# Kernel tuning notes

Hardware: AMD Instinct MI355X
Metric: run time of the kernel (lower is better)

Reference implementation:

```python
import jax, jax.numpy as jnp
import numpy as np

B, C, H, W, Q = 4, 64, 48, 48, 16384
HID = 256
IN_DIM = 4 * C + 4  # 4 pyramid levels concat + rel_coord(2) + rel_cell(2)


def _conv(x, w, b, stride=1, pad=1):
    y = jax.lax.conv_general_dilated(x, w, (stride, stride), [(pad, pad), (pad, pad)],
                                     dimension_numbers=('NCHW', 'OIHW', 'NCHW'))
    return y + b[None, :, None, None]


def _pixel_shuffle(x, r=2):
    b, c, h, w = x.shape
    return x.reshape(b, c // (r * r), r, r, h, w).transpose(0, 1, 4, 2, 5, 3).reshape(b, c // (r * r), h * r, w * r)


def _gather(img, iy, ix):
    # img [B,C,H,W], iy/ix [B,Q] int -> [B,Q,C]
    return jax.vmap(lambda f, y, x: f[:, y, x].T)(img, iy, ix)


def _nearest_idx(coord, h, w):
    # PyTorch grid_sample nearest, align_corners=False: unnormalize then nearbyint
    iy = jnp.clip(jnp.round((coord[..., 0] + 1.0) * (h / 2.0) - 0.5), 0, h - 1).astype(jnp.int32)
    ix = jnp.clip(jnp.round((coord[..., 1] + 1.0) * (w / 2.0) - 0.5), 0, w - 1).astype(jnp.int32)
    return iy, ix


def _bilinear_border(img, coord):
    b, c, h, w = img.shape
    fy = jnp.clip((coord[..., 0] + 1.0) * (h / 2.0) - 0.5, 0.0, h - 1.0)
    fx = jnp.clip((coord[..., 1] + 1.0) * (w / 2.0) - 0.5, 0.0, w - 1.0)
    y0 = jnp.floor(fy); x0 = jnp.floor(fx)
    wy = (fy - y0)[..., None]; wx = (fx - x0)[..., None]
    y0i = y0.astype(jnp.int32); x0i = x0.astype(jnp.int32)
    y1i = jnp.clip(y0i + 1, 0, h - 1); x1i = jnp.clip(x0i + 1, 0, w - 1)
    v00 = _gather(img, y0i, x0i); v01 = _gather(img, y0i, x1i)
    v10 = _gather(img, y1i, x0i); v11 = _gather(img, y1i, x1i)
    return v00 * (1 - wy) * (1 - wx) + v01 * (1 - wy) * wx + v10 * wy * (1 - wx) + v11 * wy * wx


def _mlp(x, ws, bs):
    for wm, bm in zip(ws[:-1], bs[:-1]):
        x = jnp.maximum(x @ wm + bm, 0.0)
    return x @ ws[-1] + bs[-1]


def _forward(inp, coord, cell, enc_w, enc_b, up1_w, up1_b, up2_w, up2_b, up3_w, up3_b,
             skip1_w, skip1_b, skip2_w, skip2_b, down4_w, down4_b, down5_w, down5_b,
             mlp_ws, mlp_bs):
    feat = _conv(inp, enc_w, enc_b)                                   # [B,C,H,W]
    feat_1 = _pixel_shuffle(_conv(feat, up1_w, up1_b))                # [B,C,2H,2W]
    feat_2 = _pixel_shuffle(_conv(feat_1, up2_w, up2_b))              # [B,C,4H,4W]
    feat_3 = _pixel_shuffle(_conv(feat_2, up3_w, up3_b))              # [B,C,8H,8W]
    feat_4 = _conv(feat_3, down4_w, down4_b, stride=2) + _conv(feat_2, skip1_w, skip1_b, pad=0)
    feat_5 = _conv(feat_4, down5_w, down5_b, stride=2) + _conv(feat_1, skip2_w, skip2_b, pad=0)
    h, w = feat.shape[-2], feat.shape[-1]
    rx = 1.0 / h  # 2 / h / 2
    ry = 1.0 / w
    eps_shift = 1e-6
    scale = jnp.array([h, w], dtype=coord.dtype)
    rel_cell = cell * scale
    preds, areas = [], []
    for vx in (-1.0, 1.0):
        for vy in (-1.0, 1.0):
            shift = jnp.array([vx * rx + eps_shift, vy * ry + eps_shift], dtype=coord.dtype)
            coord_ = jnp.clip(coord + shift, -1 + 1e-6, 1 - 1e-6)
            iy, ix = _nearest_idx(coord_, h, w)
            q_feat = _gather(feat, iy, ix)
            i5y, i5x = _nearest_idx(coord_, feat_5.shape[-2], feat_5.shape[-1])
            q_feat2x = _gather(feat_5, i5y, i5x)
            i4y, i4x = _nearest_idx(coord_, feat_4.shape[-2], feat_4.shape[-1])
            q_feat4x = _gather(feat_4, i4y, i4x)
            i3y, i3x = _nearest_idx(coord_, feat_3.shape[-2], feat_3.shape[-1])
            q_feat8x = _gather(feat_3, i3y, i3x)
            # feat_coord holds cell-center coords; nearest-sampling it equals this closed form
            q_coord = jnp.stack([-1.0 + (2.0 * iy + 1.0) / h, -1.0 + (2.0 * ix + 1.0) / w],
                                axis=-1).astype(coord.dtype)
            rel_coord = (coord - q_coord) * scale
            x = jnp.concatenate([q_feat, q_feat2x, q_feat4x, q_feat8x, rel_coord, rel_cell], axis=-1)
            preds.append(_mlp(x, mlp_ws, mlp_bs))
            areas.append(jnp.abs(rel_coord[..., 0] * rel_coord[..., 1]) + 1e-9)
    tot_area = areas[0] + areas[1] + areas[2] + areas[3]
    areas = [areas[3], areas[2], areas[1], areas[0]]  # local-ensemble diagonal swap
    ret = sum(p * (a / tot_area)[..., None] for p, a in zip(preds, areas))
    ret = ret + _bilinear_border(inp, coord)
    return ret


def setup_inputs() -> dict:
    key = jax.random.key(0)
    ks = jax.random.split(key, 24)
    d = {}
    d['inp'] = jax.random.normal(ks[0], (B, 3, H, W), jnp.float32)
    d['coord'] = jax.random.uniform(ks[1], (B, Q, 2), jnp.float32, -1.0, 1.0)
    d['cell'] = jnp.full((B, Q, 2), 2.0 / (8 * H), jnp.float32)

    def conv_p(k, co, ci, kh):
        wkey, _ = jax.random.split(k)
        wgt = jax.random.normal(wkey, (co, ci, kh, kh), jnp.float32) * (1.0 / np.sqrt(ci * kh * kh))
        return wgt, jnp.zeros((co,), jnp.float32)

    d['enc_w'], d['enc_b'] = conv_p(ks[2], C, 3, 3)
    d['up1_w'], d['up1_b'] = conv_p(ks[3], 4 * C, C, 3)
    d['up2_w'], d['up2_b'] = conv_p(ks[4], 4 * C, C, 3)
    d['up3_w'], d['up3_b'] = conv_p(ks[5], 4 * C, C, 3)
    d['skip1_w'], d['skip1_b'] = conv_p(ks[6], C, C, 1)
    d['skip2_w'], d['skip2_b'] = conv_p(ks[7], C, C, 1)
    d['down4_w'], d['down4_b'] = conv_p(ks[8], C, C, 3)
    d['down5_w'], d['down5_b'] = conv_p(ks[9], C, C, 3)
    dims = [IN_DIM, HID, HID, HID, HID, 3]
    for i in range(5):
        d['mlp_w%d' % i] = jax.random.normal(ks[10 + i], (dims[i], dims[i + 1]), jnp.float32) * (1.0 / np.sqrt(dims[i]))
        d['mlp_b%d' % i] = jnp.zeros((dims[i + 1],), jnp.float32)
    return d


def reference(inp, coord, cell, enc_w, enc_b, up1_w, up1_b, up2_w, up2_b, up3_w, up3_b,
              skip1_w, skip1_b, skip2_w, skip2_b, down4_w, down4_b, down5_w, down5_b,
              mlp_w0, mlp_b0, mlp_w1, mlp_b1, mlp_w2, mlp_b2, mlp_w3, mlp_b3, mlp_w4, mlp_b4):
    mlp_ws = [mlp_w0, mlp_w1, mlp_w2, mlp_w3, mlp_w4]
    mlp_bs = [mlp_b0, mlp_b1, mlp_b2, mlp_b3, mlp_b4]
    return _forward(inp, coord, cell, enc_w, enc_b, up1_w, up1_b, up2_w, up2_b, up3_w, up3_b,
                    skip1_w, skip1_b, skip2_w, skip2_b, down4_w, down4_b, down5_w, down5_b,
                    mlp_ws, mlp_bs)
```

## Files before the change

### kernel.cpp

```cpp
#include <hip/hip_runtime.h>
#include <stdint.h>

typedef unsigned int u32;
typedef unsigned short u16;

#define DI __device__ __forceinline__

DI float bf2f(u16 h){ return __uint_as_float(((u32)h)<<16); }
DI u16 f2bf(float f){ u32 u = __float_as_uint(f); return (u16)((u + 0x7FFFu + ((u>>16)&1u))>>16); }
DI u32 pack2(float a, float b){ return (u32)f2bf(a) | ((u32)f2bf(b)<<16); }

typedef __attribute__((ext_vector_type(8))) short bf16x8;
typedef __attribute__((ext_vector_type(4))) float f32x4;

#define NIN 29
__device__ const int g_in_off[NIN] = {
  0,27648,158720,289792,291520,291584,439040,439296,586752,587008,734464,
  734720,738816,738880,742976,743040,779904,779968,816832,816896,883456,
  883712,949248,949504,1015040,1015296,1080832,1081088,1081856};
#define CVT_TOTAL 1081859

#define O_INP      0
#define O_COORD    27648
#define O_CELL     158720
#define O_ENCW     289792
#define O_ENCB     291520
#define O_UP1W     291584
#define O_UP1B     439040
#define O_UP2W     439296
#define O_UP2B     586752
#define O_UP3W     587008
#define O_UP3B     734464
#define O_SK1W     734720
#define O_SK1B     738816
#define O_SK2W     738880
#define O_SK2B     742976
#define O_DN4W     743040
#define O_DN4B     779904
#define O_DN5W     779968
#define O_DN5B     816832
#define O_MLPW0    816896
#define O_MLPB0    883456
#define O_MLPW1    883712
#define O_MLPB1    949248
#define O_MLPW2    949504
#define O_MLPB2    1015040
#define O_MLPW3    1015296
#define O_MLPB3    1080832
#define O_MLPW4    1081088
#define O_MLPB4    1081856

#define W_CVT    16
#define W_FRAG   1082000
#define FG_UP1 0
#define FG_UP2 147456
#define FG_UP3 294912
#define FG_D4  442368
#define FG_D5  483328
#define CONV_FRAG_TOTAL 524288
#define FG_MLP 524288
#define FO_L0 0
#define FO_L1 73728
#define FO_L2 139264
#define FO_L3 204800
#define FO_L4 270336
#define FRAG_TOTAL 274432
#define W_FEAT   1481360
#define W_FEAT1  1776272
#define W_FEAT2  2955920
#define W_FEAT3  7674512
#define W_FEAT4  26548880
#define W_FEAT5  31267472

#define AST 296

__global__ void k_detect(const void* cell, int* flag){
  if (threadIdx.x == 0 && blockIdx.x == 0){
    u32 u = *(const u32*)cell;
    *flag = ((u >> 16) == (u & 0xFFFFu)) ? 1 : 0;
  }
}

struct Ptrs { const void* p[NIN]; };

__global__ __launch_bounds__(256) void k_convert(Ptrs ptrs, const int* __restrict__ flag, float* __restrict__ dst){
  int idx = blockIdx.x*256 + threadIdx.x;
  if (idx >= CVT_TOTAL) return;
  int bf = *flag;
  int i = 0;
  #pragma unroll
  for (int s = 1; s < NIN; ++s) if (idx >= g_in_off[s]) i = s;
  int local = idx - g_in_off[i];
  float v;
  if (bf) v = bf2f(((const u16*)ptrs.p[i])[local]);
  else    v = ((const float*)ptrs.p[i])[local];
  dst[idx] = v;
}

__global__ __launch_bounds__(256) void k_repack_conv(const float* __restrict__ cvt, u16* __restrict__ dst){
  int idx = blockIdx.x*256 + threadIdx.x;
  float v;
  if (idx < 442368){
    int seg = idx / 147456, base = idx % 147456;
    const int wo[3] = {O_UP1W, O_UP2W, O_UP3W};
    int t = base & 511, c = base >> 9;
    int j = t & 7, lane = t >> 3;
    int col = lane & 15, quad = lane >> 4;
    int kc = c >> 4, rem = c & 15;
    int wv = rem >> 2, nt = rem & 3;
    int k = kc*32 + quad*8 + j;
    int kid = k >> 6, ci = k & 63;
    int co = (wv*16 + col)*4 + nt;
    v = cvt[wo[seg] + co*576 + ci*9 + kid];
  } else {
    int x = idx - 442368;
    int seg = x / 40960, base = x % 40960;
    int t = base & 511, c = base >> 9;
    int j = t & 7, lane = t >> 3;
    int col = lane & 15, quad = lane >> 4;
    int kc = c >> 2, nt = c & 3;
    int k = kc*32 + quad*8 + j;
    int co = nt*16 + col;
    if (k < 576){
      int kid = k >> 6, ci = k & 63;
      v = cvt[(seg ? O_DN5W : O_DN4W) + co*576 + ci*9 + kid];
    } else {
      int ci = k - 576;
      v = cvt[(seg ? O_SK2W : O_SK1W) + co*64 + ci];
    }
  }
  dst[idx] = f2bf(v);
}

__global__ __launch_bounds__(256) void k_repack_mlp(const float* __restrict__ cvt, u16* __restrict__ dst){
  int idx = blockIdx.x*256 + threadIdx.x;
  int l, base;
  if (idx < FO_L1)      { l = 0; base = idx; }
  else if (idx < FO_L2) { l = 1; base = idx - FO_L1; }
  else if (idx < FO_L3) { l = 2; base = idx - FO_L2; }
  else if (idx < FO_L4) { l = 3; base = idx - FO_L3; }
  else                  { l = 4; base = idx - FO_L4; }
  int t = base & 511, c = base >> 9;
  int L = t >> 3, j = t & 7;
  int ntiles = (l == 4) ? 1 : 16;
  int kc = c / ntiles, nt = c % ntiles;
  int k = kc*32 + (L>>4)*8 + j;
  int n = nt*16 + (L&15);
  const int srcw[5] = {O_MLPW0, O_MLPW1, O_MLPW2, O_MLPW3, O_MLPW4};
  int Kvalid = (l == 0) ? 260 : 256;
  int N = (l == 4) ? 3 : 256;
  float v = 0.f;
  if (k < Kvalid && n < N) v = cvt[srcw[l] + k*N + n];
  dst[idx] = f2bf(v);
}

__global__ __launch_bounds__(256) void k_enc(const float* __restrict__ cvt, u16* __restrict__ feat){
  int gid = blockIdx.x*256 + threadIdx.x;
  int co = gid & 63, pix = gid >> 6;
  int x = pix % 48; int t = pix / 48; int y = t % 48; int b = t / 48;
  const float* w = cvt + O_ENCW + co*27;
  float acc = cvt[O_ENCB + co];
  const float* ip = cvt + O_INP + b*3*2304;
  #pragma unroll
  for (int ci = 0; ci < 3; ++ci)
    for (int dy = 0; dy < 3; ++dy){
      int iy = y + dy - 1;
      for (int dx = 0; dx < 3; ++dx){
        int ix = x + dx - 1;
        float v = (iy>=0 && iy<48 && ix>=0 && ix<48) ? ip[ci*2304 + iy*48 + ix] : 0.f;
        acc = fmaf(w[ci*9 + dy*3 + dx], v, acc);
      }
    }
  feat[pix*64 + co] = f2bf(acc);
}

template<int H>
__global__ __launch_bounds__(256,2) void k_upconv_mfma(const u16* __restrict__ in,
    const u16* __restrict__ wf, const float* __restrict__ bias, u16* __restrict__ out){
  __shared__ __align__(16) u16 patch[100*72];
  const int TW = H/8;
  int b = blockIdx.y;
  int y0 = (blockIdx.x / TW)*8, x0 = (blockIdx.x % TW)*8;
  int tid = threadIdx.x;
  if (tid < 200){
    int p = tid >> 1, half = tid & 1;
    int pr = p/10, pc = p - pr*10;
    int gy = y0+pr-1, gx = x0+pc-1;
    uint4* dst = (uint4*)((char*)(patch + p*72) + half*64);
    if (gy>=0 && gy<H && gx>=0 && gx<H){
      const uint4* src = (const uint4*)((const char*)(in + ((b*H+gy)*H+gx)*64) + half*64);
      dst[0]=src[0]; dst[1]=src[1]; dst[2]=src[2]; dst[3]=src[3];
    } else {
      uint4 z = {0,0,0,0};
      dst[0]=z; dst[1]=z; dst[2]=z; dst[3]=z;
    }
  }
  __syncthreads();
  int lane = tid & 63, wv = __builtin_amdgcn_readfirstlane(tid>>6);
  int col = lane & 15, quad = lane >> 4;
  f32x4 acc[4][4];
  #pragma unroll
  for (int nt=0;nt<4;++nt){
    float bv = bias[(wv*16+col)*4+nt];
    #pragma unroll
    for (int mt=0;mt<4;++mt) acc[mt][nt] = (f32x4){bv,bv,bv,bv};
  }
  int pyc[4], pxc[4];
  #pragma unroll
  for (int mt=0;mt<4;++mt){ int p = mt*16+col; pyc[mt]=p>>3; pxc[mt]=p&7; }
  #pragma unroll
  for (int kc=0; kc<18; ++kc){
    int dydx = kc>>1, half = kc&1;
    int dy = dydx/3, dx = dydx%3;
    bf16x8 a[4], bb[4];
    #pragma unroll
    for (int mt=0;mt<4;++mt)
      a[mt] = *(const bf16x8*)(patch + ((pyc[mt]+dy)*10 + pxc[mt]+dx)*72 + half*32 + quad*8);
    #pragma unroll
    for (int nt=0;nt<4;++nt)
      bb[nt] = *(const bf16x8*)(wf + ((kc*16 + wv*4 + nt)*64 + lane)*8);
    #pragma unroll
    for (int mt=0;mt<4;++mt)
      #pragma unroll
      for (int nt=0;nt<4;++nt)
        acc[mt][nt] = __builtin_amdgcn_mfma_f32_16x16x32_bf16(a[mt], bb[nt], acc[mt][nt], 0,0,0);
  }
  const int W2 = 2*H;
  #pragma unroll
  for (int mt=0;mt<4;++mt)
    #pragma unroll
    for (int r=0;r<4;++r){
      int p = mt*16 + quad*4 + r;
      int oy = 2*(y0 + (p>>3)), ox = 2*(x0 + (p&7));
      #pragma unroll
      for (int nt=0;nt<4;++nt)
        out[((b*W2 + oy + (nt>>1))*W2 + ox + (nt&1))*64 + wv*16 + col] = f2bf(acc[mt][nt][r]);
    }
}

template<int HO>
__global__ __launch_bounds__(256,2) void k_down_mfma(const u16* __restrict__ in3,
    const u16* __restrict__ in2, const u16* __restrict__ wf,
    const float* __restrict__ biasd, const float* __restrict__ biass, u16* __restrict__ out){
  __shared__ __align__(16) u16 patch3[289*72];
  __shared__ __align__(16) u16 patch2[64*72];
  const int HI = 2*HO, TW = HO/8;
  int b = blockIdx.y;
  int y0 = (blockIdx.x / TW)*8, x0 = (blockIdx.x % TW)*8;
  int tid = threadIdx.x;
  for (int u = tid; u < 578; u += 256){
    int p = u >> 1, half = u & 1;
    int pr = p/17, pc = p - pr*17;
    int gy = 2*y0 - 1 + pr, gx = 2*x0 - 1 + pc;
    uint4* dst = (uint4*)((char*)(patch3 + p*72) + half*64);
    if (gy>=0 && gy<HI && gx>=0 && gx<HI){
      const uint4* src = (const uint4*)((const char*)(in3 + ((b*HI+gy)*HI+gx)*64) + half*64);
      dst[0]=src[0]; dst[1]=src[1]; dst[2]=src[2]; dst[3]=src[3];
    } else { uint4 z={0,0,0,0}; dst[0]=z; dst[1]=z; dst[2]=z; dst[3]=z; }
  }
  if (tid < 128){
    int p = tid >> 1, half = tid & 1;
    int gy = y0 + (p>>3), gx = x0 + (p&7);
    uint4* dst = (uint4*)((char*)(patch2 + p*72) + half*64);
    const uint4* src = (const uint4*)((const char*)(in2 + ((b*HO+gy)*HO+gx)*64) + half*64);
    dst[0]=src[0]; dst[1]=src[1]; dst[2]=src[2]; dst[3]=src[3];
  }
  __syncthreads();
  int lane = tid & 63, wv = __builtin_amdgcn_readfirstlane(tid>>6);
  int col = lane & 15, quad = lane >> 4;
  f32x4 acc[4];
  {
    float bv = biasd[wv*16+col] + biass[wv*16+col];
    #pragma unroll
    for (int mt=0;mt<4;++mt) acc[mt] = (f32x4){bv,bv,bv,bv};
  }
  int pyc[4], pxc[4];
  #pragma unroll
  for (int mt=0;mt<4;++mt){ int p = mt*16+col; pyc[mt]=p>>3; pxc[mt]=p&7; }
  #pragma unroll
  for (int kc=0; kc<20; ++kc){
    bf16x8 a[4];
    if (kc < 18){
      int dydx = kc>>1, half = kc&1;
      int dy = dydx/3, dx = dydx%3;
      #pragma unroll
      for (int mt=0;mt<4;++mt)
        a[mt] = *(const bf16x8*)(patch3 + ((2*pyc[mt]+dy)*17 + 2*pxc[mt]+dx)*72 + half*32 + quad*8);
    } else {
      #pragma unroll
      for (int mt=0;mt<4;++mt)
        a[mt] = *(const bf16x8*)(patch2 + (pyc[mt]*8+pxc[mt])*72 + (kc-18)*32 + quad*8);
    }
    bf16x8 bb = *(const bf16x8*)(wf + ((kc*4 + wv)*64 + lane)*8);
    #pragma unroll
    for (int mt=0;mt<4;++mt)
      acc[mt] = __builtin_amdgcn_mfma_f32_16x16x32_bf16(a[mt], bb, acc[mt], 0,0,0);
  }
  #pragma unroll
  for (int mt=0;mt<4;++mt)
    #pragma unroll
    for (int r=0;r<4;++r){
      int p = mt*16 + quad*4 + r;
      out[((b*HO + y0+(p>>3))*HO + x0+(p&7))*64 + wv*16+col] = f2bf(acc[mt][r]);
    }
}

DI void shifted_coord(float cy, float cx, int e, float& cy_, float& cx_){
  float vx = (e & 2) ? 1.f : -1.f;
  float vy = (e & 1) ? 1.f : -1.f;
  float sy = (float)((double)vx*(1.0/48.0) + 1e-6);
  float sx = (float)((double)vy*(1.0/48.0) + 1e-6);
  const float clo = (float)(-1.0 + 1e-6), chi = (float)(1.0 - 1e-6);
  cy_ = fminf(fmaxf(__fadd_rn(cy, sy), clo), chi);
  cx_ = fminf(fmaxf(__fadd_rn(cx, sx), clo), chi);
}
DI int nidx(float c_, int hL){
  float f = __fadd_rn(__fmul_rn(__fadd_rn(c_, 1.f), (float)hL*0.5f), -0.5f);
  int i = (int)rintf(f);
  return max(0, min(hL-1, i));
}

template<int KC>
DI void layer_compute(const u16* __restrict__ Ab, const u16* __restrict__ wf,
                      const float* __restrict__ bias, int lane, int wv, f32x4 (&acc)[4][4]){
  int col = lane & 15, quad = lane >> 4;
  #pragma unroll
  for (int mt=0;mt<4;++mt)
    #pragma unroll
    for (int nt=0;nt<4;++nt){
      float bv = bias[wv*64 + nt*16 + col];
      acc[mt][nt] = (f32x4){bv,bv,bv,bv};
    }
  for (int kc=0; kc<KC; ++kc){
    bf16x8 a[4], b[4];
    #pragma unroll
    for (int mt=0;mt<4;++mt)
      a[mt] = *(const bf16x8*)(Ab + (mt*16+col)*AST + kc*32 + quad*8);
    #pragma unroll
    for (int nt=0;nt<4;++nt)
      b[nt] = *(const bf16x8*)(wf + ((kc*16 + wv*4 + nt)*64 + lane)*8);
    #pragma unroll
    for (int mt=0;mt<4;++mt)
      #pragma unroll
      for (int nt=0;nt<4;++nt)
        acc[mt][nt] = __builtin_amdgcn_mfma_f32_16x16x32_bf16(a[mt], b[nt], acc[mt][nt], 0, 0, 0);
  }
}

DI void layer_store(u16* __restrict__ Ab, f32x4 (&acc)[4][4], int lane, int wv){
  int col = lane & 15, quad = lane >> 4;
  #pragma unroll
  for (int mt=0;mt<4;++mt)
    #pragma unroll
    for (int nt=0;nt<4;++nt)
      #pragma unroll
      for (int r=0;r<4;++r)
        Ab[(mt*16 + quad*4 + r)*AST + wv*64 + nt*16 + col] = f2bf(fmaxf(acc[mt][nt][r], 0.f));
}

__global__ __launch_bounds__(256) void k_query(const float* __restrict__ cvt,
    const u16* __restrict__ feat, const u16* __restrict__ feat3,
    const u16* __restrict__ feat4, const u16* __restrict__ feat5,
    const u16* __restrict__ wfrag, const int* __restrict__ flagp, void* __restrict__ outv){
  __shared__ __align__(16) u16 Abuf[64*AST];
  __shared__ float predbuf[64*3];
  int tid = threadIdx.x;

  {
    int r = tid >> 2, part = tid & 3;
    int gq = blockIdx.x*16 + (r>>2);
    int e = r & 3;
    int b = gq >> 14, q = gq & 16383;
    float cy = cvt[O_COORD + (b*16384+q)*2 + 0];
    float cx = cvt[O_COORD + (b*16384+q)*2 + 1];
    float cy_, cx_; shifted_coord(cy, cx, e, cy_, cx_);
    int hL = (part==0) ? 48 : (part==1) ? 96 : (part==2) ? 192 : 384;
    const u16* fp = (part==0) ? feat : (part==1) ? feat5 : (part==2) ? feat4 : feat3;
    int iy = nidx(cy_, hL), ix = nidx(cx_, hL);
    const uint4* src = (const uint4*)(fp + ((b*hL + iy)*hL + ix)*64);
    uint4* dst = (uint4*)((char*)Abuf + r*(AST*2) + part*128);
    #pragma unroll
    for (int i=0;i<8;++i) dst[i] = src[i];
  }
  if (tid < 64){
    int gq = blockIdx.x*16 + (tid>>2);
    int e = tid & 3;
    int b = gq >> 14, q = gq & 16383;
    float cy = cvt[O_COORD + (b*16384+q)*2 + 0];
    float cx = cvt[O_COORD + (b*16384+q)*2 + 1];
    float cy_, cx_; shifted_coord(cy, cx, e, cy_, cx_);
    int iy = nidx(cy_, 48), ix = nidx(cx_, 48);
    float qy = -1.f + (2.f*iy + 1.f)*(1.f/48.f);
    float qx = -1.f + (2.f*ix + 1.f)*(1.f/48.f);
    float r0 = (cy - qy)*48.f;
    float r1 = (cx - qx)*48.f;
    float r2 = cvt[O_CELL + (b*16384+q)*2 + 0]*48.f;
    float r3 = cvt[O_CELL + (b*16384+q)*2 + 1]*48.f;
    u32* dst = (u32*)((char*)Abuf + tid*(AST*2) + 512);
    dst[0] = pack2(r0, r1);
    dst[1] = pack2(r2, r3);
    #pragma unroll
    for (int z=0; z<14; ++z) dst[2+z] = 0u;
  }
  __syncthreads();

  int lane = tid & 63;
  int wv = __builtin_amdgcn_readfirstlane(tid >> 6);

  { f32x4 acc[4][4];
    layer_compute<9>(Abuf, wfrag + FO_L0, cvt + O_MLPB0, lane, wv, acc);
    __syncthreads(); layer_store(Abuf, acc, lane, wv); }
  __syncthreads();
  { f32x4 acc[4][4];
    layer_compute<8>(Abuf, wfrag + FO_L1, cvt + O_MLPB1, lane, wv, acc);
    __syncthreads(); layer_store(Abuf, acc, lane, wv); }
  __syncthreads();
  { f32x4 acc[4][4];
    layer_compute<8>(Abuf, wfrag + FO_L2, cvt + O_MLPB2, lane, wv, acc);
    __syncthreads(); layer_store(Abuf, acc, lane, wv); }
  __syncthreads();
  { f32x4 acc[4][4];
    layer_compute<8>(Abuf, wfrag + FO_L3, cvt + O_MLPB3, lane, wv, acc);
    __syncthreads(); layer_store(Abuf, acc, lane, wv); }
  __syncthreads();

  {
    int col = lane & 15, quad = lane >> 4;
    float bv = (col < 3) ? cvt[O_MLPB4 + col] : 0.f;
    f32x4 a4 = (f32x4){bv,bv,bv,bv};
    for (int kc=0; kc<8; ++kc){
      bf16x8 av = *(const bf16x8*)(Abuf + (wv*16 + col)*AST + kc*32 + quad*8);
      bf16x8 bv8 = *(const bf16x8*)(wfrag + FO_L4 + (kc*64 + lane)*8);
      a4 = __builtin_amdgcn_mfma_f32_16x16x32_bf16(av, bv8, a4, 0, 0, 0);
    }
    if (col < 3){
      #pragma unroll
      for (int r=0;r<4;++r)
        predbuf[(wv*16 + quad*4 + r)*3 + col] = a4[r];
    }
  }
  __syncthreads();

  if (tid < 16){
    int gq = blockIdx.x*16 + tid;
    int b = gq >> 14, q = gq & 16383;
    float cy = cvt[O_COORD + (b*16384+q)*2 + 0];
    float cx = cvt[O_COORD + (b*16384+q)*2 + 1];
    float a[4];
    #pragma unroll
    for (int e=0;e<4;++e){
      float cy_, cx_; shifted_coord(cy, cx, e, cy_, cx_);
      int iy = nidx(cy_, 48), ix = nidx(cx_, 48);
      float qy = -1.f + (2.f*iy + 1.f)*(1.f/48.f);
      float qx = -1.f + (2.f*ix + 1.f)*(1.f/48.f);
      float ry = (cy - qy)*48.f, rx = (cx - qx)*48.f;
      a[e] = fabsf(ry*rx) + 1e-9f;
    }
    float tot = a[0]+a[1]+a[2]+a[3];
    float fy = fminf(fmaxf((cy+1.f)*24.f - 0.5f, 0.f), 47.f);
    float fx = fminf(fmaxf((cx+1.f)*24.f - 0.5f, 0.f), 47.f);
    float y0f = floorf(fy), x0f = floorf(fx);
    float wy = fy - y0f, wx = fx - x0f;
    int y0 = (int)y0f, x0 = (int)x0f;
    int y1 = min(y0+1, 47), x1 = min(x0+1, 47);
    int bf = *flagp;
    #pragma unroll
    for (int ch=0; ch<3; ++ch){
      const float* ip = cvt + O_INP + (b*3 + ch)*2304;
      float v00 = ip[y0*48+x0], v01 = ip[y0*48+x1], v10 = ip[y1*48+x0], v11 = ip[y1*48+x1];
      float v = v00*(1.f-wy)*(1.f-wx) + v01*(1.f-wy)*wx + v10*wy*(1.f-wx) + v11*wy*wx;
      #pragma unroll
      for (int e=0;e<4;++e)
        v += predbuf[(tid*4+e)*3 + ch] * (a[3-e]/tot);
      int oi = (b*16384+q)*3 + ch;
      if (bf) ((u16*)outv)[oi] = f2bf(v);
      else    ((float*)outv)[oi] = v;
    }
  }
}

extern "C" void kernel_launch(void* const* d_in, const int* in_sizes, int n_in,
                              void* d_out, int out_size, void* d_ws, size_t ws_size,
                              hipStream_t stream){
  float* ws = (float*)d_ws;
  int* flag = (int*)d_ws;
  float* cvt = ws + W_CVT;
  u16* frag = (u16*)(ws + W_FRAG);
  u16* feat  = (u16*)(ws + W_FEAT);
  u16* feat1 = (u16*)(ws + W_FEAT1);
  u16* feat2 = (u16*)(ws + W_FEAT2);
  u16* feat3 = (u16*)(ws + W_FEAT3);
  u16* feat4 = (u16*)(ws + W_FEAT4);
  u16* feat5 = (u16*)(ws + W_FEAT5);
  Ptrs ptrs;
  for (int i = 0; i < NIN && i < n_in; ++i) ptrs.p[i] = d_in[i];

  k_detect<<<1, 64, 0, stream>>>(d_in[2], flag);
  k_convert<<<(CVT_TOTAL+255)/256, 256, 0, stream>>>(ptrs, flag, cvt);
  k_repack_conv<<<CONV_FRAG_TOTAL/256, 256, 0, stream>>>(cvt, frag);
  k_repack_mlp<<<FRAG_TOTAL/256, 256, 0, stream>>>(cvt, frag + FG_MLP);
  k_enc<<<2304, 256, 0, stream>>>(cvt, feat);
  k_upconv_mfma<48> <<<dim3(36, 4), 256, 0, stream>>>(feat,  frag+FG_UP1, cvt+O_UP1B, feat1);
  k_upconv_mfma<96> <<<dim3(144,4), 256, 0, stream>>>(feat1, frag+FG_UP2, cvt+O_UP2B, feat2);
  k_upconv_mfma<192><<<dim3(576,4), 256, 0, stream>>>(feat2, frag+FG_UP3, cvt+O_UP3B, feat3);
  k_down_mfma<192><<<dim3(576,4), 256, 0, stream>>>(feat3, feat2, frag+FG_D4, cvt+O_DN4B, cvt+O_SK1B, feat4);
  k_down_mfma<96> <<<dim3(144,4), 256, 0, stream>>>(feat4, feat1, frag+FG_D5, cvt+O_DN5B, cvt+O_SK2B, feat5);
  k_query<<<4096, 256, 0, stream>>>(cvt, feat, feat3, feat4, feat5, frag + FG_MLP, flag, d_out);
}
```

Baseline: 433.2 us.

## Switch query MLP hidden layers to 32x32x16 MFMA and merge repack kernels

The hidden layers of the per-query MLP now use 32x32x16 bf16 MFMA tiles (2x2 per wave) in place of 16x16x32 tiles (4x4 per wave), and the MLP weight fragment layout is repacked to match. This roughly halves the LDS A-fragment and global B-fragment loads per MFMA and cuts the instruction count. The conv and MLP repack kernels are merged into one launch to save a kernel launch. The risk is a different accumulator register footprint and a more scattered LDS store pattern in the new layer store.

```diff
diff --git a/kernel.cpp b/kernel.cpp
--- a/kernel.cpp
+++ b/kernel.cpp
@@ -12,6 +12,7 @@
 
 typedef __attribute__((ext_vector_type(8))) short bf16x8;
 typedef __attribute__((ext_vector_type(4))) float f32x4;
+typedef __attribute__((ext_vector_type(16))) float f32x16;
 
 #define NIN 29
 __device__ const int g_in_off[NIN] = {
@@ -65,6 +66,7 @@
 #define FO_L3 204800
 #define FO_L4 270336
 #define FRAG_TOTAL 274432
+#define REPACK_TOTAL (CONV_FRAG_TOTAL + FRAG_TOTAL)
 #define W_FEAT   1481360
 #define W_FEAT1  1776272
 #define W_FEAT2  2955920
@@ -97,7 +99,7 @@
   dst[idx] = v;
 }
 
-__global__ __launch_bounds__(256) void k_repack_conv(const float* __restrict__ cvt, u16* __restrict__ dst){
+__global__ __launch_bounds__(256) void k_repack_all(const float* __restrict__ cvt, u16* __restrict__ dst){
   int idx = blockIdx.x*256 + threadIdx.x;
   float v;
   if (idx < 442368){
@@ -112,7 +114,7 @@
     int kid = k >> 6, ci = k & 63;
     int co = (wv*16 + col)*4 + nt;
     v = cvt[wo[seg] + co*576 + ci*9 + kid];
-  } else {
+  } else if (idx < CONV_FRAG_TOTAL){
     int x = idx - 442368;
     int seg = x / 40960, base = x % 40960;
     int t = base & 511, c = base >> 9;
@@ -128,29 +130,31 @@
       int ci = k - 576;
       v = cvt[(seg ? O_SK2W : O_SK1W) + co*64 + ci];
     }
-  }
-  dst[idx] = f2bf(v);
-}
-
-__global__ __launch_bounds__(256) void k_repack_mlp(const float* __restrict__ cvt, u16* __restrict__ dst){
-  int idx = blockIdx.x*256 + threadIdx.x;
-  int l, base;
-  if (idx < FO_L1)      { l = 0; base = idx; }
-  else if (idx < FO_L2) { l = 1; base = idx - FO_L1; }
-  else if (idx < FO_L3) { l = 2; base = idx - FO_L2; }
-  else if (idx < FO_L4) { l = 3; base = idx - FO_L3; }
-  else                  { l = 4; base = idx - FO_L4; }
-  int t = base & 511, c = base >> 9;
-  int L = t >> 3, j = t & 7;
-  int ntiles = (l == 4) ? 1 : 16;
-  int kc = c / ntiles, nt = c % ntiles;
-  int k = kc*32 + (L>>4)*8 + j;
-  int n = nt*16 + (L&15);
-  const int srcw[5] = {O_MLPW0, O_MLPW1, O_MLPW2, O_MLPW3, O_MLPW4};
-  int Kvalid = (l == 0) ? 260 : 256;
-  int N = (l == 4) ? 3 : 256;
-  float v = 0.f;
-  if (k < Kvalid && n < N) v = cvt[srcw[l] + k*N + n];
+  } else {
+    int midx = idx - FG_MLP;
+    int l, base;
+    if (midx < FO_L1)      { l = 0; base = midx; }
+    else if (midx < FO_L2) { l = 1; base = midx - FO_L1; }
+    else if (midx < FO_L3) { l = 2; base = midx - FO_L2; }
+    else if (midx < FO_L4) { l = 3; base = midx - FO_L3; }
+    else                   { l = 4; base = midx - FO_L4; }
+    int t = base & 511, c = base >> 9;
+    int L = t >> 3, j = t & 7;
+    int k, n;
+    if (l < 4){
+      int kc = c >> 3, nt2 = c & 7;
+      k = kc*16 + (L>>5)*8 + j;
+      n = nt2*32 + (L&31);
+    } else {
+      k = c*32 + (L>>4)*8 + j;
+      n = L & 15;
+    }
+    const int srcw[5] = {O_MLPW0, O_MLPW1, O_MLPW2, O_MLPW3, O_MLPW4};
+    int Kvalid = (l == 0) ? 260 : 256;
+    int N = (l == 4) ? 3 : 256;
+    v = 0.f;
+    if (k < Kvalid && n < N) v = cvt[srcw[l] + k*N + n];
+  }
   dst[idx] = f2bf(v);
 }
 
@@ -320,42 +324,45 @@
   return max(0, min(hL-1, i));
 }
 
-template<int KC>
-DI void layer_compute(const u16* __restrict__ Ab, const u16* __restrict__ wf,
-                      const float* __restrict__ bias, int lane, int wv, f32x4 (&acc)[4][4]){
-  int col = lane & 15, quad = lane >> 4;
-  #pragma unroll
-  for (int mt=0;mt<4;++mt)
-    #pragma unroll
-    for (int nt=0;nt<4;++nt){
-      float bv = bias[wv*64 + nt*16 + col];
-      acc[mt][nt] = (f32x4){bv,bv,bv,bv};
-    }
-  for (int kc=0; kc<KC; ++kc){
-    bf16x8 a[4], b[4];
-    #pragma unroll
-    for (int mt=0;mt<4;++mt)
-      a[mt] = *(const bf16x8*)(Ab + (mt*16+col)*AST + kc*32 + quad*8);
-    #pragma unroll
-    for (int nt=0;nt<4;++nt)
-      b[nt] = *(const bf16x8*)(wf + ((kc*16 + wv*4 + nt)*64 + lane)*8);
-    #pragma unroll
-    for (int mt=0;mt<4;++mt)
-      #pragma unroll
-      for (int nt=0;nt<4;++nt)
-        acc[mt][nt] = __builtin_amdgcn_mfma_f32_16x16x32_bf16(a[mt], b[nt], acc[mt][nt], 0, 0, 0);
-  }
-}
-
-DI void layer_store(u16* __restrict__ Ab, f32x4 (&acc)[4][4], int lane, int wv){
-  int col = lane & 15, quad = lane >> 4;
-  #pragma unroll
-  for (int mt=0;mt<4;++mt)
-    #pragma unroll
-    for (int nt=0;nt<4;++nt)
-      #pragma unroll
-      for (int r=0;r<4;++r)
-        Ab[(mt*16 + quad*4 + r)*AST + wv*64 + nt*16 + col] = f2bf(fmaxf(acc[mt][nt][r], 0.f));
+template<int KC16>
+DI void layer_compute32(const u16* __restrict__ Ab, const u16* __restrict__ wf,
+                        const float* __restrict__ bias, int lane, int wv, f32x16 (&acc)[2][2]){
+  int col = lane & 31, half = lane >> 5;
+  #pragma unroll
+  for (int mt=0;mt<2;++mt)
+    #pragma unroll
+    for (int nt=0;nt<2;++nt){
+      float bv = bias[wv*64 + nt*32 + col];
+      #pragma unroll
+      for (int r=0;r<16;++r) acc[mt][nt][r] = bv;
+    }
+  for (int kc=0; kc<KC16; ++kc){
+    bf16x8 a[2], b[2];
+    #pragma unroll
+    for (int mt=0;mt<2;++mt)
+      a[mt] = *(const bf16x8*)(Ab + (mt*32+col)*AST + kc*16 + half*8);
+    #pragma unroll
+    for (int nt=0;nt<2;++nt)
+      b[nt] = *(const bf16x8*)(wf + ((kc*8 + wv*2 + nt)*64 + lane)*8);
+    #pragma unroll
+    for (int mt=0;mt<2;++mt)
+      #pragma unroll
+      for (int nt=0;nt<2;++nt)
+        acc[mt][nt] = __builtin_amdgcn_mfma_f32_32x32x16_bf16(a[mt], b[nt], acc[mt][nt], 0, 0, 0);
+  }
+}
+
+DI void layer_store32(u16* __restrict__ Ab, f32x16 (&acc)[2][2], int lane, int wv){
+  int col = lane & 31, half = lane >> 5;
+  #pragma unroll
+  for (int mt=0;mt<2;++mt)
+    #pragma unroll
+    for (int nt=0;nt<2;++nt)
+      #pragma unroll
+      for (int r=0;r<16;++r){
+        int row = mt*32 + (r&3) + 8*(r>>2) + 4*half;
+        Ab[row*AST + wv*64 + nt*32 + col] = f2bf(fmaxf(acc[mt][nt][r], 0.f));
+      }
 }
 
 __global__ __launch_bounds__(256) void k_query(const float* __restrict__ cvt,
@@ -407,21 +414,21 @@
   int lane = tid & 63;
   int wv = __builtin_amdgcn_readfirstlane(tid >> 6);
 
-  { f32x4 acc[4][4];
-    layer_compute<9>(Abuf, wfrag + FO_L0, cvt + O_MLPB0, lane, wv, acc);
-    __syncthreads(); layer_store(Abuf, acc, lane, wv); }
-  __syncthreads();
-  { f32x4 acc[4][4];
-    layer_compute<8>(Abuf, wfrag + FO_L1, cvt + O_MLPB1, lane, wv, acc);
-    __syncthreads(); layer_store(Abuf, acc, lane, wv); }
-  __syncthreads();
-  { f32x4 acc[4][4];
-    layer_compute<8>(Abuf, wfrag + FO_L2, cvt + O_MLPB2, lane, wv, acc);
-    __syncthreads(); layer_store(Abuf, acc, lane, wv); }
-  __syncthreads();
-  { f32x4 acc[4][4];
-    layer_compute<8>(Abuf, wfrag + FO_L3, cvt + O_MLPB3, lane, wv, acc);
-    __syncthreads(); layer_store(Abuf, acc, lane, wv); }
+  { f32x16 acc[2][2];
+    layer_compute32<18>(Abuf, wfrag + FO_L0, cvt + O_MLPB0, lane, wv, acc);
+    __syncthreads(); layer_store32(Abuf, acc, lane, wv); }
+  __syncthreads();
+  { f32x16 acc[2][2];
+    layer_compute32<16>(Abuf, wfrag + FO_L1, cvt + O_MLPB1, lane, wv, acc);
+    __syncthreads(); layer_store32(Abuf, acc, lane, wv); }
+  __syncthreads();
+  { f32x16 acc[2][2];
+    layer_compute32<16>(Abuf, wfrag + FO_L2, cvt + O_MLPB2, lane, wv, acc);
+    __syncthreads(); layer_store32(Abuf, acc, lane, wv); }
+  __syncthreads();
+  { f32x16 acc[2][2];
+    layer_compute32<16>(Abuf, wfrag + FO_L3, cvt + O_MLPB3, lane, wv, acc);
+    __syncthreads(); layer_store32(Abuf, acc, lane, wv); }
   __syncthreads();
 
   {
@@ -497,8 +504,7 @@
 
   k_detect<<<1, 64, 0, stream>>>(d_in[2], flag);
   k_convert<<<(CVT_TOTAL+255)/256, 256, 0, stream>>>(ptrs, flag, cvt);
-  k_repack_conv<<<CONV_FRAG_TOTAL/256, 256, 0, stream>>>(cvt, frag);
-  k_repack_mlp<<<FRAG_TOTAL/256, 256, 0, stream>>>(cvt, frag + FG_MLP);
+  k_repack_all<<<REPACK_TOTAL/256, 256, 0, stream>>>(cvt, frag);
   k_enc<<<2304, 256, 0, stream>>>(cvt, feat);
   k_upconv_mfma<48> <<<dim3(36, 4), 256, 0, stream>>>(feat,  frag+FG_UP1, cvt+O_UP1B, feat1);
   k_upconv_mfma<96> <<<dim3(144,4), 256, 0, stream>>>(feat1, frag+FG_UP2, cvt+O_UP2B, feat2);
```

Result: slower. 454.9 us (+5.0%).

## Merge setup kernels and permute upconv weights for vectorized pixel-shuffle stores

Applied to the files above, without the earlier changes.

Drops the separate detect kernel by checking the bf16 flag inline from the cell input, and folds the two weight-repack kernels into one launch. The upconv weight fragments are permuted so each lane owns four consecutive output channels of one sub-pixel, letting the pixel-shuffle epilogue write packed 8-byte stores instead of scattered 2-byte stores. This cuts launch overhead and store transactions, and in exchange each thread of k_convert and k_query now reads the cell word itself.

```diff
diff --git a/kernel.cpp b/kernel.cpp
--- a/kernel.cpp
+++ b/kernel.cpp
@@ -9,6 +9,7 @@
 DI float bf2f(u16 h){ return __uint_as_float(((u32)h)<<16); }
 DI u16 f2bf(float f){ u32 u = __float_as_uint(f); return (u16)((u + 0x7FFFu + ((u>>16)&1u))>>16); }
 DI u32 pack2(float a, float b){ return (u32)f2bf(a) | ((u32)f2bf(b)<<16); }
+DI int is_bf16(const void* p){ u32 u = *(const u32*)p; return ((u>>16) == (u & 0xFFFFu)) ? 1 : 0; }
 
 typedef __attribute__((ext_vector_type(8))) short bf16x8;
 typedef __attribute__((ext_vector_type(4))) float f32x4;
@@ -65,6 +66,7 @@
 #define FO_L3 204800
 #define FO_L4 270336
 #define FRAG_TOTAL 274432
+#define REPACK_TOTAL (CONV_FRAG_TOTAL + FRAG_TOTAL)
 #define W_FEAT   1481360
 #define W_FEAT1  1776272
 #define W_FEAT2  2955920
@@ -74,19 +76,12 @@
 
 #define AST 296
 
-__global__ void k_detect(const void* cell, int* flag){
-  if (threadIdx.x == 0 && blockIdx.x == 0){
-    u32 u = *(const u32*)cell;
-    *flag = ((u >> 16) == (u & 0xFFFFu)) ? 1 : 0;
-  }
-}
-
 struct Ptrs { const void* p[NIN]; };
 
-__global__ __launch_bounds__(256) void k_convert(Ptrs ptrs, const int* __restrict__ flag, float* __restrict__ dst){
+__global__ __launch_bounds__(256) void k_convert(Ptrs ptrs, float* __restrict__ dst){
   int idx = blockIdx.x*256 + threadIdx.x;
   if (idx >= CVT_TOTAL) return;
-  int bf = *flag;
+  int bf = is_bf16(ptrs.p[2]);
   int i = 0;
   #pragma unroll
   for (int s = 1; s < NIN; ++s) if (idx >= g_in_off[s]) i = s;
@@ -97,7 +92,7 @@
   dst[idx] = v;
 }
 
-__global__ __launch_bounds__(256) void k_repack_conv(const float* __restrict__ cvt, u16* __restrict__ dst){
+__global__ __launch_bounds__(256) void k_repack_all(const float* __restrict__ cvt, u16* __restrict__ dst){
   int idx = blockIdx.x*256 + threadIdx.x;
   float v;
   if (idx < 442368){
@@ -110,9 +105,9 @@
     int wv = rem >> 2, nt = rem & 3;
     int k = kc*32 + quad*8 + j;
     int kid = k >> 6, ci = k & 63;
-    int co = (wv*16 + col)*4 + nt;
+    int co = (wv*16 + (col>>2)*4 + nt)*4 + (col&3);
     v = cvt[wo[seg] + co*576 + ci*9 + kid];
-  } else {
+  } else if (idx < CONV_FRAG_TOTAL){
     int x = idx - 442368;
     int seg = x / 40960, base = x % 40960;
     int t = base & 511, c = base >> 9;
@@ -128,29 +123,26 @@
       int ci = k - 576;
       v = cvt[(seg ? O_SK2W : O_SK1W) + co*64 + ci];
     }
-  }
-  dst[idx] = f2bf(v);
-}
-
-__global__ __launch_bounds__(256) void k_repack_mlp(const float* __restrict__ cvt, u16* __restrict__ dst){
-  int idx = blockIdx.x*256 + threadIdx.x;
-  int l, base;
-  if (idx < FO_L1)      { l = 0; base = idx; }
-  else if (idx < FO_L2) { l = 1; base = idx - FO_L1; }
-  else if (idx < FO_L3) { l = 2; base = idx - FO_L2; }
-  else if (idx < FO_L4) { l = 3; base = idx - FO_L3; }
-  else                  { l = 4; base = idx - FO_L4; }
-  int t = base & 511, c = base >> 9;
-  int L = t >> 3, j = t & 7;
-  int ntiles = (l == 4) ? 1 : 16;
-  int kc = c / ntiles, nt = c % ntiles;
-  int k = kc*32 + (L>>4)*8 + j;
-  int n = nt*16 + (L&15);
-  const int srcw[5] = {O_MLPW0, O_MLPW1, O_MLPW2, O_MLPW3, O_MLPW4};
-  int Kvalid = (l == 0) ? 260 : 256;
-  int N = (l == 4) ? 3 : 256;
-  float v = 0.f;
-  if (k < Kvalid && n < N) v = cvt[srcw[l] + k*N + n];
+  } else {
+    int midx = idx - FG_MLP;
+    int l, base;
+    if (midx < FO_L1)      { l = 0; base = midx; }
+    else if (midx < FO_L2) { l = 1; base = midx - FO_L1; }
+    else if (midx < FO_L3) { l = 2; base = midx - FO_L2; }
+    else if (midx < FO_L4) { l = 3; base = midx - FO_L3; }
+    else                   { l = 4; base = midx - FO_L4; }
+    int t = base & 511, c = base >> 9;
+    int L = t >> 3, j = t & 7;
+    int ntiles = (l == 4) ? 1 : 16;
+    int kc = c / ntiles, nt = c % ntiles;
+    int k = kc*32 + (L>>4)*8 + j;
+    int n = nt*16 + (L&15);
+    const int srcw[5] = {O_MLPW0, O_MLPW1, O_MLPW2, O_MLPW3, O_MLPW4};
+    int Kvalid = (l == 0) ? 260 : 256;
+    int N = (l == 4) ? 3 : 256;
+    v = 0.f;
+    if (k < Kvalid && n < N) v = cvt[srcw[l] + k*N + n];
+  }
   dst[idx] = f2bf(v);
 }
 
@@ -198,10 +190,12 @@
   __syncthreads();
   int lane = tid & 63, wv = __builtin_amdgcn_readfirstlane(tid>>6);
   int col = lane & 15, quad = lane >> 4;
+  int rs = col & 3;
+  int c2b = wv*16 + (col>>2)*4;
   f32x4 acc[4][4];
   #pragma unroll
   for (int nt=0;nt<4;++nt){
-    float bv = bias[(wv*16+col)*4+nt];
+    float bv = bias[(c2b + nt)*4 + rs];
     #pragma unroll
     for (int mt=0;mt<4;++mt) acc[mt][nt] = (f32x4){bv,bv,bv,bv};
   }
@@ -231,10 +225,11 @@
     #pragma unroll
     for (int r=0;r<4;++r){
       int p = mt*16 + quad*4 + r;
-      int oy = 2*(y0 + (p>>3)), ox = 2*(x0 + (p&7));
-      #pragma unroll
-      for (int nt=0;nt<4;++nt)
-        out[((b*W2 + oy + (nt>>1))*W2 + ox + (nt&1))*64 + wv*16 + col] = f2bf(acc[mt][nt][r]);
+      int oy = 2*(y0 + (p>>3)) + (rs>>1), ox = 2*(x0 + (p&7)) + (rs&1);
+      uint2 v2;
+      v2.x = pack2(acc[mt][0][r], acc[mt][1][r]);
+      v2.y = pack2(acc[mt][2][r], acc[mt][3][r]);
+      *(uint2*)(out + ((b*W2 + oy)*W2 + ox)*64 + c2b) = v2;
     }
 }
 
@@ -361,7 +356,7 @@
 __global__ __launch_bounds__(256) void k_query(const float* __restrict__ cvt,
     const u16* __restrict__ feat, const u16* __restrict__ feat3,
     const u16* __restrict__ feat4, const u16* __restrict__ feat5,
-    const u16* __restrict__ wfrag, const int* __restrict__ flagp, void* __restrict__ outv){
+    const u16* __restrict__ wfrag, const void* __restrict__ cellraw, void* __restrict__ outv){
   __shared__ __align__(16) u16 Abuf[64*AST];
   __shared__ float predbuf[64*3];
   int tid = threadIdx.x;
@@ -463,7 +458,7 @@
     float wy = fy - y0f, wx = fx - x0f;
     int y0 = (int)y0f, x0 = (int)x0f;
     int y1 = min(y0+1, 47), x1 = min(x0+1, 47);
-    int bf = *flagp;
+    int bf = is_bf16(cellraw);
     #pragma unroll
     for (int ch=0; ch<3; ++ch){
       const float* ip = cvt + O_INP + (b*3 + ch)*2304;
@@ -483,7 +478,6 @@
                               void* d_out, int out_size, void* d_ws, size_t ws_size,
                               hipStream_t stream){
   float* ws = (float*)d_ws;
-  int* flag = (int*)d_ws;
   float* cvt = ws + W_CVT;
   u16* frag = (u16*)(ws + W_FRAG);
   u16* feat  = (u16*)(ws + W_FEAT);
@@ -495,15 +489,13 @@
   Ptrs ptrs;
   for (int i = 0; i < NIN && i < n_in; ++i) ptrs.p[i] = d_in[i];
 
-  k_detect<<<1, 64, 0, stream>>>(d_in[2], flag);
-  k_convert<<<(CVT_TOTAL+255)/256, 256, 0, stream>>>(ptrs, flag, cvt);
-  k_repack_conv<<<CONV_FRAG_TOTAL/256, 256, 0, stream>>>(cvt, frag);
-  k_repack_mlp<<<FRAG_TOTAL/256, 256, 0, stream>>>(cvt, frag + FG_MLP);
+  k_convert<<<(CVT_TOTAL+255)/256, 256, 0, stream>>>(ptrs, cvt);
+  k_repack_all<<<REPACK_TOTAL/256, 256, 0, stream>>>(cvt, frag);
   k_enc<<<2304, 256, 0, stream>>>(cvt, feat);
   k_upconv_mfma<48> <<<dim3(36, 4), 256, 0, stream>>>(feat,  frag+FG_UP1, cvt+O_UP1B, feat1);
   k_upconv_mfma<96> <<<dim3(144,4), 256, 0, stream>>>(feat1, frag+FG_UP2, cvt+O_UP2B, feat2);
   k_upconv_mfma<192><<<dim3(576,4), 256, 0, stream>>>(feat2, frag+FG_UP3, cvt+O_UP3B, feat3);
   k_down_mfma<192><<<dim3(576,4), 256, 0, stream>>>(feat3, feat2, frag+FG_D4, cvt+O_DN4B, cvt+O_SK1B, feat4);
   k_down_mfma<96> <<<dim3(144,4), 256, 0, stream>>>(feat4, feat1, frag+FG_D5, cvt+O_DN5B, cvt+O_SK2B, feat5);
-  k_query<<<4096, 256, 0, stream>>>(cvt, feat, feat3, feat4, feat5, frag + FG_MLP, flag, d_out);
-}
+  k_query<<<4096, 256, 0, stream>>>(cvt, feat, feat3, feat4, feat5, frag + FG_MLP, d_in[2], d_out);
+}
```

Result: faster. 399.2 us (-7.8%).
